# Performance work log

Hardware: AMD Instinct MI355X
Metric: run time of the kernel (lower is better)

The kernel has to match this reference:

```python
import jax, jax.numpy as jnp
import numpy as np

B, N, R, S, H, D, HIDDEN = 4, 1028, 4, 32, 12, 64, 32
L = (2 * S - 1) ** 2  # 3969 relative-position bins


def _build_tables():
    # CPB relative-coordinate table (signed log1p-normalized offsets)
    rng = np.arange(-(S - 1), S, dtype=np.float32)
    dY, dX = np.meshgrid(rng, rng, indexing='ij')
    rel = np.stack([dY / max(S - 1, 1), dX / max(S - 1, 1)], -1).reshape(-1, 2)
    rel_table = np.sign(rel) * np.log1p(np.abs(rel))  # [L, 2]
    # 2D relative-position index table over the SxS patch grid
    Y, X = np.meshgrid(np.arange(S), np.arange(S), indexing='ij')
    flat = np.stack([Y, X], 0).reshape(2, -1)          # [2, P]
    d = flat[:, :, None] - flat[:, None, :]            # [2, P, P]
    d = np.transpose(d, (1, 2, 0)).copy()              # [P, P, 2]
    d[:, :, 0] += S - 1
    d[:, :, 1] += S - 1
    d[:, :, 0] *= 2 * S - 1
    l_idx = d.sum(-1)                                  # [P, P] in [0, L)
    idx = np.full((N, N), -1, dtype=np.int64)          # -1 sentinel for register tokens
    idx[R:, R:] = l_idx
    return jnp.asarray(rel_table, jnp.float32), jnp.asarray(idx)


def setup_inputs() -> dict:
    key = jax.random.key(0)
    ks = jax.random.split(key, 8)
    rel_table, idx_table = _build_tables()
    return {
        'q': jax.random.normal(ks[0], (B, H, N, D), jnp.float32),
        'k': jax.random.normal(ks[1], (B, H, N, D), jnp.float32),
        'v': jax.random.normal(ks[2], (B, H, N, D), jnp.float32),
        'mu': jax.random.normal(ks[3], (B, 2 * H, N), jnp.float32),
        'rel_table': rel_table,                              # [L, 2] buffer
        'W1': jax.random.normal(ks[4], (HIDDEN, 2), jnp.float32) * 0.5,
        'b1': jax.random.normal(ks[5], (HIDDEN,), jnp.float32) * 0.1,
        'W2': jax.random.normal(ks[6], (H, HIDDEN), jnp.float32) * 0.05,
        'gamma': jax.random.normal(ks[7], (H,), jnp.float32),
        'idx_table': idx_table,                              # [N, N] int64
    }


def reference(q, k, v, mu, rel_table, W1, b1, W2, gamma, idx_table):
    # CPB MLP: Linear(2->hidden) + exact GELU + Linear(hidden->H, no bias)
    hid = jax.nn.gelu(rel_table @ W1.T + b1, approximate=False)   # [L, HIDDEN]
    bt = hid @ W2.T                                               # [L, H]
    bt_ext = jnp.concatenate([jnp.zeros((1, H), bt.dtype), bt], 0)  # [L+1, H]
    bias = bt_ext[idx_table + 1]                                  # [N, N, H]; sentinel -1 -> zero row

    # per-token gates: signed log1p transform then q-side + k-side split
    mu_t = jnp.sign(mu) * jnp.log1p(jnp.abs(mu))                  # [B, 2H, N]
    mu_q, mu_k = mu_t[:, :H], mu_t[:, H:]                         # each [B, H, N]
    g = mu_q[:, :, :, None] + mu_k[:, :, None, :]                 # [B, H, N, N]
    gam = jax.nn.sigmoid(gamma)[None, :, None, None]              # [1, H, 1, 1]

    scale = 1.0 / jnp.sqrt(jnp.asarray(D, jnp.float32))
    scores = jnp.einsum('bhqd,bhkd->bhqk', q, k) * scale
    scores = scores + gam * g * jnp.transpose(bias, (2, 0, 1))[None]  # [B, H, N, N]
    attn = jax.nn.softmax(scores, axis=-1)
    return jnp.einsum('bhqk,bhkd->bhqd', attn, v)
```

## Files before the change

kernel.cpp:

```cpp
#include <hip/hip_runtime.h>

#define B_ 4
#define H_ 12
#define N_ 1028
#define D_ 64
#define R_ 4
#define L_ 3969
#define HID_ 32
#define KBLK 64
#define NT_ 17
#define NBH_ 48
#define QBLK 128
#define NQT 9
#define NWG (NBH_*NQT)
#define TBL 3973
#define LOG2E 1.4426950408889634f
#define SCL1 (0.125f*LOG2E)

typedef __attribute__((ext_vector_type(8)))  short bf16x8;
typedef __attribute__((ext_vector_type(4)))  float f32x4;
typedef __attribute__((ext_vector_type(2)))  unsigned int u32x2;
typedef __attribute__((ext_vector_type(4)))  unsigned int u32x4;
typedef __attribute__((address_space(3))) unsigned int lds_u32;
typedef const __attribute__((address_space(1))) unsigned int glb_u32;

__device__ __forceinline__ unsigned pkbf(float lo, float hi) {
  unsigned r;
  asm("v_cvt_pk_bf16_f32 %0, %1, %2" : "=v"(r) : "v"(lo), "v"(hi));
  return r;
}
__device__ __forceinline__ float exp2_fast(float x) {
  float r; asm("v_exp_f32 %0, %1" : "=v"(r) : "v"(x)); return r;
}
__device__ __forceinline__ float sgnlog1p(float x) {
  float t = log1pf(fabsf(x));
  return (x > 0.f) ? t : ((x < 0.f) ? -t : 0.f);
}

__global__ __launch_bounds__(256) void prep_kernel(
    const float* __restrict__ rel, const float* __restrict__ W1,
    const float* __restrict__ b1, const float* __restrict__ W2,
    const float* __restrict__ gammag, const float* __restrict__ kg,
    const float* __restrict__ vg, const float* __restrict__ mug,
    float* __restrict__ btgf, float* __restrict__ mut,
    unsigned short* __restrict__ kv)
{
  const int blk = blockIdx.x, tid = threadIdx.x;
  if (blk < 16) {
    if (blk == 0 && tid < 48) btgf[(tid >> 2)*TBL + (tid & 3)] = 0.f;
    int l = blk*256 + tid;
    if (l < L_) {
      float r0 = rel[2*l], r1 = rel[2*l+1];
      float hid[HID_];
#pragma unroll
      for (int j = 0; j < HID_; ++j) {
        float x = W1[2*j]*r0 + W1[2*j+1]*r1 + b1[j];
        hid[j] = 0.5f * x * (1.f + erff(x * 0.70710678118654752f));
      }
#pragma unroll
      for (int h = 0; h < H_; ++h) {
        float acc = 0.f;
#pragma unroll
        for (int j = 0; j < HID_; ++j) acc += W2[h*HID_+j]*hid[j];
        float gscl = LOG2E / (1.f + __expf(-gammag[h]));
        btgf[h*TBL + 4 + l] = gscl * acc;
      }
    }
  } else if (blk < 16 + NBH_*NT_) {
    const int idx = blk - 16;
    const int bh = idx / NT_, t = idx - bh*NT_;
    const int k0 = t * KBLK;
    const float* kb = kg + (size_t)bh*N_*D_;
    const float* vb = vg + (size_t)bh*N_*D_;
    unsigned short* Ko = kv + (size_t)idx*8192;
    unsigned short* Vo = Ko + 4096;
    const int kcb = tid >> 4, d4 = (tid & 15)*4;
#pragma unroll
    for (int i = 0; i < 4; ++i) {
      int kc = kcb + i*16;
      int kr = k0 + kc; if (kr >= N_) kr = N_-1;
      f32x4 a = *(const f32x4*)(kb + (size_t)kr*D_ + d4);
      *(u32x2*)&Ko[kc*64 + (d4 ^ ((kc & 7) << 3))] = (u32x2){pkbf(a[0],a[1]), pkbf(a[2],a[3])};
    }
    const int vd0 = (tid >> 4)*4, vkc0 = (tid & 15)*4;
    const int loc = vkc0 & 31;
    const int p0 = 32*(vkc0 >> 5) + 8*((loc >> 2) & 3) + 4*(loc >> 4);
    f32x4 r[4];
#pragma unroll
    for (int i = 0; i < 4; ++i) {
      int kr = k0 + vkc0 + i; if (kr >= N_) kr = N_-1;
      r[i] = *(const f32x4*)(vb + (size_t)kr*D_ + vd0);
    }
#pragma unroll
    for (int j = 0; j < 4; ++j) {
      int d = vd0 + j;
      int addr = d*64 + ((p0 & 56) ^ ((d & 7) << 3)) + (p0 & 7);
      *(u32x2*)&Vo[addr] = (u32x2){pkbf(r[0][j],r[1][j]), pkbf(r[2][j],r[3][j])};
    }
  } else {
    int idx = (blk - (16 + NBH_*NT_))*256 + tid;
    if (idx < NBH_*N_) {
      int bh = idx / N_, n = idx - bh*N_;
      int b = bh / H_, h = bh - b*H_;
      mut[idx] = sgnlog1p(mug[((size_t)b*2*H_ + H_ + h)*N_ + n]);
    }
  }
}

__global__ __launch_bounds__(512, 4) void attn_kernel(
    const float* __restrict__ qg, const float* __restrict__ mug,
    const float* __restrict__ btgf, const float* __restrict__ mut,
    const unsigned short* __restrict__ kv, float* __restrict__ outg)
{
  __shared__ __align__(16) unsigned short KV[2][8192];
  __shared__ __align__(16) float btgs[TBL];

  const int tid = threadIdx.x;
  const int w = tid >> 6, lane = tid & 63, g = lane >> 4, c = lane & 15;

  const int orig = blockIdx.x;
  const int wg = (orig & 7)*(NWG/8) + (orig >> 3);
  const int bh = wg / NQT;
  const int qt = wg - bh*NQT;
  const int b = bh / H_, h = bh - b*H_;
  const int q0 = qt * QBLK;

  const float* qb = qg + (size_t)bh*N_*D_;
  const float* mt = mut + (size_t)bh*N_;
  const unsigned short* kvb = kv + (size_t)bh*NT_*8192;

  {
    const float* bth = btgf + h*TBL;
    for (int i = tid; i < TBL; i += 512) btgs[i] = bth[i];
  }

  const int qrow = q0 + 16*w + c;
  const int qrc = qrow < N_ ? qrow : N_-1;
  bf16x8 qf[2];
#pragma unroll
  for (int ch = 0; ch < 2; ++ch) {
    const float* p = qb + (size_t)qrc*D_ + ch*32 + 8*g;
    f32x4 a0 = *(const f32x4*)p;
    f32x4 a1 = *(const f32x4*)(p + 4);
    u32x4 qw;
    qw[0] = pkbf(a0[0]*SCL1, a0[1]*SCL1); qw[1] = pkbf(a0[2]*SCL1, a0[3]*SCL1);
    qw[2] = pkbf(a1[0]*SCL1, a1[1]*SCL1); qw[3] = pkbf(a1[2]*SCL1, a1[3]*SCL1);
    qf[ch] = __builtin_bit_cast(bf16x8, qw);
  }
  const float muq_c = (qrow < N_) ? sgnlog1p(mug[((size_t)b*2*H_ + h)*N_ + qrow]) : 0.f;
  const int qi = qrow - R_;
  const bool qok = (qi >= 0) && (qrow < N_);
  const int qy = qi >> 5, qx = qi & 31;
  const int lqc = qy*63 + qx + 1988;

  auto issue = [&](int tt, int pp) {
    const char* src = (const char*)(kvb + (size_t)tt*8192) + w*2048;
    char* dst = (char*)&KV[pp][0] + w*2048;
#pragma unroll
    for (int j = 0; j < 2; ++j) {
      int o = j*1024;
      __builtin_amdgcn_global_load_lds((glb_u32*)(src + o + lane*16),
                                       (lds_u32*)(dst + o), 16, 0, 0);
    }
  };

  float mrun = -3.0e38f, lrun = 0.f;
  f32x4 O[4];
#pragma unroll
  for (int dt = 0; dt < 4; ++dt) O[dt] = (f32x4){0.f,0.f,0.f,0.f};

  issue(0, 0);

  for (int t = 0; t < NT_; ++t) {
    const int k0 = t * KBLK;
    const int p = t & 1;

    asm volatile("s_waitcnt vmcnt(0)" ::: "memory");
    __syncthreads();

    f32x4 mk4[4];
#pragma unroll
    for (int kt = 0; kt < 4; ++kt) {
      int mb = k0 + kt*16 + 4*g;
      mb = mb > 1024 ? 1024 : mb;
      mk4[kt] = *(const f32x4*)&mt[mb];
    }
    __builtin_amdgcn_sched_barrier(0);
    if (t + 1 < NT_) issue(t + 1, p ^ 1);

    const unsigned short* Kl = &KV[p][0];
    const unsigned short* Vl = &KV[p][4096];

    f32x4 sc[4];
#pragma unroll
    for (int kt = 0; kt < 4; ++kt) {
      int row = kt*16 + c;
      int sw = (row & 7) << 3;
      bf16x8 ka0 = *(const bf16x8*)&Kl[row*64 + ((8*g) ^ sw)];
      bf16x8 ka1 = *(const bf16x8*)&Kl[row*64 + ((32 + 8*g) ^ sw)];
      f32x4 s = (f32x4){0.f,0.f,0.f,0.f};
      s = __builtin_amdgcn_mfma_f32_16x16x32_bf16(ka0, qf[0], s, 0, 0, 0);
      s = __builtin_amdgcn_mfma_f32_16x16x32_bf16(ka1, qf[1], s, 0, 0, 0);
      sc[kt] = s;
    }

    float smax = -3.0e38f;
#pragma unroll
    for (int kt = 0; kt < 4; ++kt) {
      const f32x4 mk = mk4[kt];
      int ki0 = k0 + kt*16 + 4*g - R_;
      int lk = (ki0 >> 5)*63 + (ki0 & 31);
      int va = lqc - lk;
      bool okq = ((unsigned)ki0 < 1024u) && qok;
      int basep = okq ? va : 3;
      f32x4 bv;
      bv[0] = btgs[basep-3]; bv[1] = btgs[basep-2];
      bv[2] = btgs[basep-1]; bv[3] = btgs[basep];
      bool mq = (ki0 < 1024);
      f32x4 s = sc[kt];
#pragma unroll
      for (int r = 0; r < 4; ++r) {
        float val = s[r] + (muq_c + mk[r]) * bv[3-r];
        val = mq ? val : -3.0e38f;
        s[r] = val;
        smax = fmaxf(smax, val);
      }
      sc[kt] = s;
    }
    smax = fmaxf(smax, __shfl_xor(smax, 16));
    smax = fmaxf(smax, __shfl_xor(smax, 32));

    if (__any(smax > mrun)) {
      float mnew = fmaxf(mrun, smax);
      float corr = exp2_fast(mrun - mnew);
      lrun *= corr;
#pragma unroll
      for (int dt = 0; dt < 4; ++dt)
#pragma unroll
        for (int r = 0; r < 4; ++r) O[dt][r] *= corr;
      mrun = mnew;
    }

    float psum = 0.f;
#pragma unroll
    for (int kt = 0; kt < 4; ++kt)
#pragma unroll
      for (int r = 0; r < 4; ++r) {
        float pv = exp2_fast(sc[kt][r] - mrun);
        sc[kt][r] = pv;
        psum += pv;
      }
    psum += __shfl_xor(psum, 16);
    psum += __shfl_xor(psum, 32);
    lrun += psum;

    u32x4 pa[2];
#pragma unroll
    for (int kh = 0; kh < 2; ++kh) {
      pa[kh][0] = pkbf(sc[2*kh][0],   sc[2*kh][1]);
      pa[kh][1] = pkbf(sc[2*kh][2],   sc[2*kh][3]);
      pa[kh][2] = pkbf(sc[2*kh+1][0], sc[2*kh+1][1]);
      pa[kh][3] = pkbf(sc[2*kh+1][2], sc[2*kh+1][3]);
    }

#pragma unroll
    for (int kh = 0; kh < 2; ++kh) {
      bf16x8 pfr = __builtin_bit_cast(bf16x8, pa[kh]);
      int sw = (c & 7) << 3;
#pragma unroll
      for (int dt = 0; dt < 4; ++dt) {
        int d = dt*16 + c;
        bf16x8 va = *(const bf16x8*)&Vl[d*64 + ((32*kh + 8*g) ^ sw)];
        O[dt] = __builtin_amdgcn_mfma_f32_16x16x32_bf16(va, pfr, O[dt], 0, 0, 0);
      }
    }
  }

  float rlv = 1.f / lrun;
  const int qo = q0 + 16*w + c;
  if (qo < N_) {
    float* ob = outg + ((size_t)bh*N_ + qo)*64;
#pragma unroll
    for (int dt = 0; dt < 4; ++dt) {
      f32x4 ov;
#pragma unroll
      for (int r = 0; r < 4; ++r) ov[r] = O[dt][r] * rlv;
      *(f32x4*)(ob + dt*16 + 4*g) = ov;
    }
  }
}

extern "C" void kernel_launch(void* const* d_in, const int* in_sizes, int n_in,
                              void* d_out, int out_size, void* d_ws, size_t ws_size,
                              hipStream_t stream) {
  const float* q     = (const float*)d_in[0];
  const float* k     = (const float*)d_in[1];
  const float* v     = (const float*)d_in[2];
  const float* mu    = (const float*)d_in[3];
  const float* rel   = (const float*)d_in[4];
  const float* W1    = (const float*)d_in[5];
  const float* b1    = (const float*)d_in[6];
  const float* W2    = (const float*)d_in[7];
  const float* gamma = (const float*)d_in[8];

  char* wsb = (char*)d_ws;
  float* btgf = (float*)wsb;
  float* mut  = (float*)(wsb + 190704);
  unsigned short* kvimg = (unsigned short*)(wsb + 388080);

  const int prep_blocks = 16 + NBH_*NT_ + (NBH_*N_ + 255)/256;
  prep_kernel<<<dim3(prep_blocks), dim3(256), 0, stream>>>(rel, W1, b1, W2, gamma,
                                                           k, v, mu, btgf, mut, kvimg);
  attn_kernel<<<dim3(NWG), dim3(512), 0, stream>>>(q, mu, btgf, mut, kvimg,
                                                   (float*)d_out);
}
```

Before: 59.64 us.

## Stage k-side mu gates in LDS, peel masked last tile, raise occupancy hint

The per-tile global loads of k-side mu gate values are replaced by a one-time copy of the whole row of gates into shared memory, so the loop reads them from LDS instead of issuing global loads behind a sched barrier. The masking of out-of-range keys is peeled into a separate path for the final tile, letting the other tiles skip the select. Launch bounds are raised to 6 waves per SIMD, which caps registers more tightly. The extra LDS buffer and the tighter register budget may cause spills or limit occupancy.

Result: no change. 59.37 us (-0.5%).

```diff
diff --git a/kernel.cpp b/kernel.cpp
--- a/kernel.cpp
+++ b/kernel.cpp
@@ -14,6 +14,7 @@
 #define NQT 9
 #define NWG (NBH_*NQT)
 #define TBL 3973
+#define MUKP 1088
 #define LOG2E 1.4426950408889634f
 #define SCL1 (0.125f*LOG2E)
 
@@ -107,13 +108,14 @@
   }
 }
 
-__global__ __launch_bounds__(512, 4) void attn_kernel(
+__global__ __launch_bounds__(512, 6) void attn_kernel(
     const float* __restrict__ qg, const float* __restrict__ mug,
     const float* __restrict__ btgf, const float* __restrict__ mut,
     const unsigned short* __restrict__ kv, float* __restrict__ outg)
 {
   __shared__ __align__(16) unsigned short KV[2][8192];
   __shared__ __align__(16) float btgs[TBL];
+  __shared__ __align__(16) float muks[MUKP];
 
   const int tid = threadIdx.x;
   const int w = tid >> 6, lane = tid & 63, g = lane >> 4, c = lane & 15;
@@ -126,12 +128,13 @@
   const int q0 = qt * QBLK;
 
   const float* qb = qg + (size_t)bh*N_*D_;
-  const float* mt = mut + (size_t)bh*N_;
   const unsigned short* kvb = kv + (size_t)bh*NT_*8192;
 
   {
     const float* bth = btgf + h*TBL;
     for (int i = tid; i < TBL; i += 512) btgs[i] = bth[i];
+    const float* mt = mut + (size_t)bh*N_;
+    for (int i = tid; i < MUKP; i += 512) muks[i] = mt[i < N_ ? i : N_-1];
   }
 
   const int qrow = q0 + 16*w + c;
@@ -177,15 +180,6 @@
 
     asm volatile("s_waitcnt vmcnt(0)" ::: "memory");
     __syncthreads();
-
-    f32x4 mk4[4];
-#pragma unroll
-    for (int kt = 0; kt < 4; ++kt) {
-      int mb = k0 + kt*16 + 4*g;
-      mb = mb > 1024 ? 1024 : mb;
-      mk4[kt] = *(const f32x4*)&mt[mb];
-    }
-    __builtin_amdgcn_sched_barrier(0);
     if (t + 1 < NT_) issue(t + 1, p ^ 1);
 
     const unsigned short* Kl = &KV[p][0];
@@ -205,27 +199,50 @@
     }
 
     float smax = -3.0e38f;
-#pragma unroll
-    for (int kt = 0; kt < 4; ++kt) {
-      const f32x4 mk = mk4[kt];
-      int ki0 = k0 + kt*16 + 4*g - R_;
-      int lk = (ki0 >> 5)*63 + (ki0 & 31);
-      int va = lqc - lk;
-      bool okq = ((unsigned)ki0 < 1024u) && qok;
-      int basep = okq ? va : 3;
-      f32x4 bv;
-      bv[0] = btgs[basep-3]; bv[1] = btgs[basep-2];
-      bv[2] = btgs[basep-1]; bv[3] = btgs[basep];
-      bool mq = (ki0 < 1024);
-      f32x4 s = sc[kt];
-#pragma unroll
-      for (int r = 0; r < 4; ++r) {
-        float val = s[r] + (muq_c + mk[r]) * bv[3-r];
-        val = mq ? val : -3.0e38f;
-        s[r] = val;
-        smax = fmaxf(smax, val);
-      }
-      sc[kt] = s;
+    if (t < NT_-1) {
+#pragma unroll
+      for (int kt = 0; kt < 4; ++kt) {
+        const f32x4 mk = *(const f32x4*)&muks[k0 + kt*16 + 4*g];
+        int ki0 = k0 + kt*16 + 4*g - R_;
+        int lk = (ki0 >> 5)*63 + (ki0 & 31);
+        int va = lqc - lk;
+        bool okq = (ki0 >= 0) && qok;
+        int basep = okq ? va : 3;
+        f32x4 bv;
+        bv[0] = btgs[basep-3]; bv[1] = btgs[basep-2];
+        bv[2] = btgs[basep-1]; bv[3] = btgs[basep];
+        f32x4 s = sc[kt];
+#pragma unroll
+        for (int r = 0; r < 4; ++r) {
+          float val = s[r] + (muq_c + mk[r]) * bv[3-r];
+          s[r] = val;
+          smax = fmaxf(smax, val);
+        }
+        sc[kt] = s;
+      }
+    } else {
+#pragma unroll
+      for (int kt = 0; kt < 4; ++kt) {
+        const f32x4 mk = *(const f32x4*)&muks[k0 + kt*16 + 4*g];
+        int ki0 = k0 + kt*16 + 4*g - R_;
+        int lk = (ki0 >> 5)*63 + (ki0 & 31);
+        int va = lqc - lk;
+        bool okq = ((unsigned)ki0 < 1024u) && qok;
+        int basep = okq ? va : 3;
+        f32x4 bv;
+        bv[0] = btgs[basep-3]; bv[1] = btgs[basep-2];
+        bv[2] = btgs[basep-1]; bv[3] = btgs[basep];
+        bool mq = (ki0 < 1024);
+        f32x4 s = sc[kt];
+#pragma unroll
+        for (int r = 0; r < 4; ++r) {
+          float val = s[r] + (muq_c + mk[r]) * bv[3-r];
+          val = mq ? val : -3.0e38f;
+          s[r] = val;
+          smax = fmaxf(smax, val);
+        }
+        sc[kt] = s;
+      }
     }
     smax = fmaxf(smax, __shfl_xor(smax, 16));
     smax = fmaxf(smax, __shfl_xor(smax, 32));
```
